# Kernel tuning notes

Measured on AMD Instinct MI355X. Metric: run time of the kernel, lower is better.

## Reference

```python
import jax, jax.numpy as jnp
import numpy as np

B, S, D = 16, 1024, 768
H = 12
HD = D // H  # 64


def setup_inputs() -> dict:
    key = jax.random.key(0)
    ks = jax.random.split(key, 9)
    s = 1.0 / np.sqrt(D)
    x = jax.random.normal(ks[0], (B, S, D), dtype=jnp.float32)
    Wq = jax.random.uniform(ks[1], (H, HD, D), minval=-s, maxval=s, dtype=jnp.float32)
    bq = jax.random.uniform(ks[2], (H, HD), minval=-s, maxval=s, dtype=jnp.float32)
    Wk = jax.random.uniform(ks[3], (H, HD, D), minval=-s, maxval=s, dtype=jnp.float32)
    bk = jax.random.uniform(ks[4], (H, HD), minval=-s, maxval=s, dtype=jnp.float32)
    Wv = jax.random.uniform(ks[5], (H, HD, D), minval=-s, maxval=s, dtype=jnp.float32)
    bv = jax.random.uniform(ks[6], (H, HD), minval=-s, maxval=s, dtype=jnp.float32)
    Wo = jax.random.uniform(ks[7], (D, D), minval=-s, maxval=s, dtype=jnp.float32)
    bo = jax.random.uniform(ks[8], (D,), minval=-s, maxval=s, dtype=jnp.float32)
    return {"x": x, "Wq": Wq, "bq": bq, "Wk": Wk, "bk": bk,
            "Wv": Wv, "bv": bv, "Wo": Wo, "bo": bo}


def reference(x, Wq, bq, Wk, bk, Wv, bv, Wo, bo):
    # per-head projections: [B,S,D] x [H,HD,D] -> [B,H,S,HD]
    q = jnp.einsum('bsd,hed->bhse', x, Wq) + bq[None, :, None, :]
    k = jnp.einsum('bsd,hed->bhse', x, Wk) + bk[None, :, None, :]
    v = jnp.einsum('bsd,hed->bhse', x, Wv) + bv[None, :, None, :]
    scores = jnp.einsum('bhse,bhte->bhst', q, k) / jnp.sqrt(jnp.float32(HD))
    weights = jax.nn.softmax(scores, axis=-1)  # [B,H,S,S]
    attn = jnp.einsum('bhst,bhte->bhse', weights, v)  # [B,H,S,HD]
    # concat heads along last dim (head order matches torch.cat)
    concat = attn.transpose(0, 2, 1, 3).reshape(B, S, H * HD)
    out = concat @ Wo.T + bo
    return out
```

## Files before the change

kernel.cpp:

```cpp
#include <hip/hip_runtime.h>
#include <hip/hip_bf16.h>

typedef unsigned short u16;
typedef unsigned int u32;
typedef __attribute__((ext_vector_type(2))) unsigned int u32x2;
typedef __attribute__((ext_vector_type(4))) unsigned int u32x4;
typedef __attribute__((ext_vector_type(4))) float f32x4;
typedef __attribute__((ext_vector_type(16))) float f32x16;
typedef __attribute__((ext_vector_type(8))) short s16x8;
typedef __attribute__((ext_vector_type(4))) unsigned short u16x4;
typedef __attribute__((ext_vector_type(8))) unsigned short u16x8;

#define QSCALE 0.18033688011112042f

#define BARRIER() do { __builtin_amdgcn_s_barrier(); __builtin_amdgcn_sched_barrier(0); } while (0)
#define WAIT_VM0() do { asm volatile("s_waitcnt vmcnt(0)" ::: "memory"); __builtin_amdgcn_sched_barrier(0); } while (0)

__device__ inline u16 f2bf(float f) {
  union { float f; unsigned u; } x; x.f = f;
  unsigned r = x.u + 0x7FFFu + ((x.u >> 16) & 1u);
  return (u16)(r >> 16);
}

__device__ inline u32 cvtpk(float lo, float hi) {
  u32 r;
  asm("v_cvt_pk_bf16_f32 %0, %1, %2" : "=v"(r) : "v"(lo), "v"(hi));
  return r;
}

__device__ inline void pl32swap(u32& a, u32& b) {
  asm("v_permlane32_swap_b32 %0, %1" : "+v"(a), "+v"(b));
}

__global__ void cvt_all(const float* __restrict__ x,
                        const float* __restrict__ Wq, const float* __restrict__ Wk,
                        const float* __restrict__ Wv, const float* __restrict__ Wo,
                        const float* __restrict__ bq, const float* __restrict__ bk,
                        const float* __restrict__ bv,
                        u16* __restrict__ xb, u16* __restrict__ wqkv,
                        u16* __restrict__ wo, float* __restrict__ bqkv) {
  int i = blockIdx.x * blockDim.x + threadIdx.x;
  const int NX = 3145728;
  const int NW = 147456;
  if (i < NX) {
    const float4 v = ((const float4*)x)[i];
    u16x4 o; o[0] = f2bf(v.x); o[1] = f2bf(v.y); o[2] = f2bf(v.z); o[3] = f2bf(v.w);
    ((u16x4*)xb)[i] = o;
    return;
  }
  i -= NX;
  if (i < 4 * NW) {
    const int w = i / NW, k = i - w * NW;
    const float* s = (w == 0) ? Wq : (w == 1) ? Wk : (w == 2) ? Wv : Wo;
    u16* d = (w == 3) ? wo : wqkv + (size_t)w * 589824;
    const float4 v = ((const float4*)s)[k];
    u16x4 o; o[0] = f2bf(v.x); o[1] = f2bf(v.y); o[2] = f2bf(v.z); o[3] = f2bf(v.w);
    ((u16x4*)d)[k] = o;
    return;
  }
  i -= 4 * NW;
  if (i < 576) {
    const int w = i / 192, k = i - w * 192;
    const float* s = (w == 0) ? bq : (w == 1) ? bk : bv;
    ((float4*)bqkv)[w * 192 + k] = ((const float4*)s)[k];
  }
}

template<int FC, int STORE_BF16, int QKV_SCALE, int WV>
__global__ __launch_bounds__(512, 2) void gemm8(
    const u16* __restrict__ A, const u16* __restrict__ Bm,
    const float* __restrict__ bias, void* __restrict__ C,
    u16* __restrict__ vt,
    int N, int K, int ntiles)
{
  constexpr int ASZ = 32768;
  constexpr int BSZ = FC * 8192;
  constexpr int BUF = ASZ + BSZ;
  __shared__ char lds[2 * BUF];

  const int tid = threadIdx.x, wave = tid >> 6, lane = tid & 63;
  const int il = lane & 15, g = lane >> 4;
  const int Lr = lane >> 3, Lc = lane & 7;
  const int wm = wave >> 2, wn = wave & 3;

  const int cpx = (int)gridDim.x >> 3;
  const int orig = (blockIdx.x & 7) * cpx + (blockIdx.x >> 3);
  const int tm = (orig / ntiles) * 256, tn = (orig % ntiles) * (FC * 64);

  const size_t Kb = (size_t)K * 2;
  const int colb = (Lc * 16) ^ (Lr << 4);

  auto stageAll = [&](int buf, int k0) {
    char* base = &lds[buf * BUF];
#pragma unroll
    for (int c = 0; c < 4; ++c) {
      const int row = tm + c * 64 + wave * 8 + Lr;
      const char* src = (const char*)A + (size_t)row * Kb + k0 * 2 + colb;
      __builtin_amdgcn_global_load_lds((const __attribute__((address_space(1))) void*)src,
          (__attribute__((address_space(3))) void*)(base + c * 8192 + wave * 1024), 16, 0, 0);
    }
#pragma unroll
    for (int c = 0; c < FC; ++c) {
      const int row = tn + c * 64 + wave * 8 + Lr;
      const char* src = (const char*)Bm + (size_t)row * Kb + k0 * 2 + colb;
      __builtin_amdgcn_global_load_lds((const __attribute__((address_space(1))) void*)src,
          (__attribute__((address_space(3))) void*)(base + ASZ + c * 8192 + wave * 1024), 16, 0, 0);
    }
  };
  auto ldA = [&](int buf, int fr, int kk) -> s16x8 {
    const int row = wm * 128 + fr * 16 + il;
    const int cb = (kk * 64 + g * 16) ^ ((il & 7) << 4);
    return *(const s16x8*)&lds[buf * BUF + row * 128 + cb];
  };
  auto ldB = [&](int buf, int fc, int kk) -> s16x8 {
    const int row = wn * (FC * 16) + fc * 16 + il;
    const int cb = (kk * 64 + g * 16) ^ ((il & 7) << 4);
    return *(const s16x8*)&lds[buf * BUF + ASZ + row * 128 + cb];
  };

  f32x4 acc[8][FC] = {};
  const int nK = K >> 6;

  stageAll(0, 0);
  WAIT_VM0();
  BARRIER();

  for (int t = 0; t < nK; ++t) {
    const int cur = t & 1;
    const bool pf = (t + 1 < nK);
    if (pf) stageAll(cur ^ 1, (t + 1) << 6);

    s16x8 bfr[FC][2];
#pragma unroll
    for (int fc = 0; fc < FC; ++fc) { bfr[fc][0] = ldB(cur, fc, 0); bfr[fc][1] = ldB(cur, fc, 1); }

#pragma unroll
    for (int p = 0; p < 4; ++p) {
      s16x8 a00 = ldA(cur, 2 * p, 0),     a01 = ldA(cur, 2 * p, 1);
      s16x8 a10 = ldA(cur, 2 * p + 1, 0), a11 = ldA(cur, 2 * p + 1, 1);
      __builtin_amdgcn_s_setprio(1);
#pragma unroll
      for (int fc = 0; fc < FC; ++fc) {
        acc[2*p][fc]   = __builtin_amdgcn_mfma_f32_16x16x32_bf16(a00, bfr[fc][0], acc[2*p][fc], 0, 0, 0);
        acc[2*p][fc]   = __builtin_amdgcn_mfma_f32_16x16x32_bf16(a01, bfr[fc][1], acc[2*p][fc], 0, 0, 0);
        acc[2*p+1][fc] = __builtin_amdgcn_mfma_f32_16x16x32_bf16(a10, bfr[fc][0], acc[2*p+1][fc], 0, 0, 0);
        acc[2*p+1][fc] = __builtin_amdgcn_mfma_f32_16x16x32_bf16(a11, bfr[fc][1], acc[2*p+1][fc], 0, 0, 0);
      }
      __builtin_amdgcn_s_setprio(0);
    }
    if (pf) WAIT_VM0();
    BARRIER();
  }

  if (WV && tn >= 1536) {
#pragma unroll
    for (int fr = 0; fr < 8; ++fr) {
      const int row0 = tm + wm * 128 + fr * 16 + g * 4;
      const int bb_ = row0 >> 10, s0 = row0 & 1023;
#pragma unroll
      for (int fc = 0; fc < FC; ++fc) {
        const int hcol = tn + wn * (FC * 16) + fc * 16 + il - 1536;
        const float bb = bias[hcol + 1536];
        u16x4 o;
#pragma unroll
        for (int r = 0; r < 4; ++r) o[r] = f2bf(acc[fr][fc][r] + bb);
        *(u16x4*)(vt + ((size_t)(bb_ * 12 + (hcol >> 6)) * 64 + (hcol & 63)) * 1024 + s0) = o;
      }
    }
    return;
  }
#pragma unroll
  for (int fr = 0; fr < 8; ++fr) {
    const int row0 = tm + wm * 128 + fr * 16 + g * 4;
#pragma unroll
    for (int fc = 0; fc < FC; ++fc) {
      const int col = tn + wn * (FC * 16) + fc * 16 + il;
      const float bb = bias[col];
#pragma unroll
      for (int r = 0; r < 4; ++r) {
        float v = acc[fr][fc][r] + bb;
        if (QKV_SCALE) { if (col < 768) v *= QSCALE; }
        if (STORE_BF16) ((u16*)C)[(size_t)(row0 + r) * N + col] = f2bf(v);
        else            ((float*)C)[(size_t)(row0 + r) * N + col] = v;
      }
    }
  }
}

__global__ __launch_bounds__(256) void attn_fwd(const u16* __restrict__ qkv,
                                                const u16* __restrict__ vT,
                                                u16* __restrict__ concat)
{
  __shared__ u16 Kl[64 * 64];
  __shared__ u16 Vl[64 * 64];

  const int tid = threadIdx.x, wave = tid >> 6, lane = tid & 63;
  const int wg = blockIdx.x;
  const int bh = (wg & 7) | ((wg >> 6) << 3);
  const int qb = (wg >> 3) & 7;
  const int b = bh / 12, h = bh % 12;
  const int q = lane & 31, hi = lane >> 5;
  const int qs0 = qb * 128 + wave * 32;

  const char* qkvB = (const char*)qkv;
  const size_t rowB = (size_t)b * 1024 * 4608;
  const char* vtB = (const char*)vT + (size_t)bh * 64 * 2048;

  s16x8 qf[4];
  {
    const char* qp = qkvB + rowB + (size_t)(qs0 + q) * 4608 + h * 128 + hi * 16;
#pragma unroll
    for (int s = 0; s < 4; ++s) qf[s] = *(const s16x8*)(qp + s * 32);
  }

  float l_ = 0.f;
  f32x16 accO[2] = {};

  const int Lr = lane >> 3, Lc = lane & 7;
  const int colb = (Lc * 16) ^ ((Lr & 7) << 4);
  const int swk = (q & 7) << 4;

  for (int kv0 = 0; kv0 < 1024; kv0 += 64) {
#pragma unroll
    for (int i = 0; i < 2; ++i) {
      const int row = wave * 16 + i * 8 + Lr;
      const char* ks = qkvB + rowB + (size_t)(kv0 + row) * 4608 + 1536 + h * 128 + colb;
      __builtin_amdgcn_global_load_lds((const __attribute__((address_space(1))) void*)ks,
          (__attribute__((address_space(3))) void*)(Kl + (wave * 16 + i * 8) * 64), 16, 0, 0);
      const char* vs = vtB + (size_t)row * 2048 + kv0 * 2 + colb;
      __builtin_amdgcn_global_load_lds((const __attribute__((address_space(1))) void*)vs,
          (__attribute__((address_space(3))) void*)(Vl + (wave * 16 + i * 8) * 64), 16, 0, 0);
    }
    __syncthreads();

    f32x16 st[2] = {};
    __builtin_amdgcn_s_setprio(1);
#pragma unroll
    for (int s = 0; s < 4; ++s) {
      const int cb = (s * 32 + hi * 16) ^ swk;
      s16x8 k0 = *(const s16x8*)((const char*)Kl + q * 128 + cb);
      s16x8 k1 = *(const s16x8*)((const char*)Kl + (32 + q) * 128 + cb);
      st[0] = __builtin_amdgcn_mfma_f32_32x32x16_bf16(k0, qf[s], st[0], 0, 0, 0);
      st[1] = __builtin_amdgcn_mfma_f32_32x32x16_bf16(k1, qf[s], st[1], 0, 0, 0);
    }
    __builtin_amdgcn_s_setprio(0);

    float cs0 = 0.f, cs1 = 0.f;
#pragma unroll
    for (int r = 0; r < 16; ++r) {
      const float p0 = __builtin_amdgcn_exp2f(st[0][r]);
      const float p1 = __builtin_amdgcn_exp2f(st[1][r]);
      st[0][r] = p0; st[1][r] = p1;
      cs0 += p0; cs1 += p1;
    }
    l_ += cs0 + cs1;

    s16x8 pa[4];
#pragma unroll
    for (int kb = 0; kb < 2; ++kb)
#pragma unroll
      for (int ks = 0; ks < 2; ++ks) {
        u32 A0 = cvtpk(st[kb][ks * 8 + 0], st[kb][ks * 8 + 1]);
        u32 A1 = cvtpk(st[kb][ks * 8 + 2], st[kb][ks * 8 + 3]);
        u32 B0 = cvtpk(st[kb][ks * 8 + 4], st[kb][ks * 8 + 5]);
        u32 B1 = cvtpk(st[kb][ks * 8 + 6], st[kb][ks * 8 + 7]);
        pl32swap(A0, B0);
        pl32swap(A1, B1);
        u32x4 w = {A0, A1, B0, B1};
        pa[kb * 2 + ks] = __builtin_bit_cast(s16x8, w);
      }

    __builtin_amdgcn_s_setprio(1);
#pragma unroll
    for (int ksub = 0; ksub < 4; ++ksub) {
      const int cb = (ksub * 32 + hi * 16) ^ swk;
      s16x8 v0 = *(const s16x8*)((const char*)Vl + q * 128 + cb);
      s16x8 v1 = *(const s16x8*)((const char*)Vl + (32 + q) * 128 + cb);
      accO[0] = __builtin_amdgcn_mfma_f32_32x32x16_bf16(v0, pa[ksub], accO[0], 0, 0, 0);
      accO[1] = __builtin_amdgcn_mfma_f32_32x32x16_bf16(v1, pa[ksub], accO[1], 0, 0, 0);
    }
    __builtin_amdgcn_s_setprio(0);
    __syncthreads();
  }

  l_ += __shfl_xor(l_, 32);
  const float linv = __builtin_amdgcn_rcpf(l_);
  u16* crow = concat + ((size_t)b * 1024 + qs0 + q) * 768 + h * 64;
#pragma unroll
  for (int eb = 0; eb < 2; ++eb)
#pragma unroll
    for (int rq = 0; rq < 4; ++rq) {
      u32 w0 = cvtpk(accO[eb][rq * 4 + 0] * linv, accO[eb][rq * 4 + 1] * linv);
      u32 w1 = cvtpk(accO[eb][rq * 4 + 2] * linv, accO[eb][rq * 4 + 3] * linv);
      u32x2 w = {w0, w1};
      *(u16x4*)(crow + eb * 32 + rq * 8 + hi * 4) = __builtin_bit_cast(u16x4, w);
    }
}

extern "C" void kernel_launch(void* const* d_in, const int* in_sizes, int n_in,
                              void* d_out, int out_size, void* d_ws, size_t ws_size,
                              hipStream_t stream) {
  const float* x  = (const float*)d_in[0];
  const float* Wq = (const float*)d_in[1];
  const float* bq = (const float*)d_in[2];
  const float* Wk = (const float*)d_in[3];
  const float* bk = (const float*)d_in[4];
  const float* Wv = (const float*)d_in[5];
  const float* bv = (const float*)d_in[6];
  const float* Wo = (const float*)d_in[7];
  const float* bo = (const float*)d_in[8];

  const size_t XN = (size_t)16384 * 768;
  const size_t WN = (size_t)768 * 768;

  u16* xb   = (u16*)d_ws;
  u16* wqkv = xb + XN;
  u16* wo   = wqkv + 3 * WN;
  float* bqkv = (float*)(wo + WN);
  u16* qkv  = (u16*)(bqkv + 2304);
  u16* vt   = qkv + (size_t)16384 * 2304;
  u16* cc   = xb;

  cvt_all<<<(3736128 + 255) / 256, 256, 0, stream>>>(
      x, Wq, Wk, Wv, Wo, bq, bk, bv, xb, wqkv, wo, bqkv);

  gemm8<3, 1, 1, 1><<<768, 512, 0, stream>>>(xb, wqkv, bqkv, qkv, vt, 2304, 768, 12);

  attn_fwd<<<1536, 256, 0, stream>>>(qkv, vt, cc);

  gemm8<3, 0, 0, 0><<<256, 512, 0, stream>>>(cc, wo, bo, d_out, nullptr, 768, 768, 4);
}
```

Before: 182.0 us.

## Switch attention to 16x16 MFMA tiles with LDS-staged P and more workgroups

Rewrites the attention kernel so each wave owns 16 query rows instead of 32, using 16x16x32 bf16 MFMAs instead of 32x32x16. The P matrix now goes through a per-wave LDS buffer rather than being rearranged with permlane32 swaps, and the grid doubles to 3072 workgroups with a remapped block index and launch bounds asking for 8 blocks per CU. The goal is lower register use and higher occupancy so latency is better hidden. The cost is that K/V tiles are loaded twice as often per query, plus extra LDS traffic and round trips for P.

Result: slower. 189.1 us (+3.9%).

```diff
diff --git a/kernel.cpp b/kernel.cpp
--- a/kernel.cpp
+++ b/kernel.cpp
@@ -26,10 +26,6 @@
   u32 r;
   asm("v_cvt_pk_bf16_f32 %0, %1, %2" : "=v"(r) : "v"(lo), "v"(hi));
   return r;
-}
-
-__device__ inline void pl32swap(u32& a, u32& b) {
-  asm("v_permlane32_swap_b32 %0, %1" : "+v"(a), "+v"(b));
 }
 
 __global__ void cvt_all(const float* __restrict__ x,
@@ -187,38 +183,40 @@
   }
 }
 
-__global__ __launch_bounds__(256) void attn_fwd(const u16* __restrict__ qkv,
-                                                const u16* __restrict__ vT,
-                                                u16* __restrict__ concat)
+__global__ __launch_bounds__(256, 8) void attn_fwd(const u16* __restrict__ qkv,
+                                                   const u16* __restrict__ vT,
+                                                   u16* __restrict__ concat)
 {
   __shared__ u16 Kl[64 * 64];
   __shared__ u16 Vl[64 * 64];
+  __shared__ u16 Pl[4][16 * 64];
 
   const int tid = threadIdx.x, wave = tid >> 6, lane = tid & 63;
   const int wg = blockIdx.x;
-  const int bh = (wg & 7) | ((wg >> 6) << 3);
-  const int qb = (wg >> 3) & 7;
+  const int orig = (wg & 7) * 384 + (wg >> 3);
+  const int bh = orig >> 4, qb = orig & 15;
   const int b = bh / 12, h = bh % 12;
-  const int q = lane & 31, hi = lane >> 5;
-  const int qs0 = qb * 128 + wave * 32;
+  const int il = lane & 15, g = lane >> 4;
+  const int qs0 = qb * 64 + wave * 16;
 
   const char* qkvB = (const char*)qkv;
   const size_t rowB = (size_t)b * 1024 * 4608;
   const char* vtB = (const char*)vT + (size_t)bh * 64 * 2048;
-
-  s16x8 qf[4];
+  char* PlB = (char*)&Pl[wave][0];
+
+  s16x8 qf0, qf1;
   {
-    const char* qp = qkvB + rowB + (size_t)(qs0 + q) * 4608 + h * 128 + hi * 16;
-#pragma unroll
-    for (int s = 0; s < 4; ++s) qf[s] = *(const s16x8*)(qp + s * 32);
+    const char* qp = qkvB + rowB + (size_t)(qs0 + il) * 4608 + h * 128 + g * 16;
+    qf0 = *(const s16x8*)qp;
+    qf1 = *(const s16x8*)(qp + 64);
   }
 
   float l_ = 0.f;
-  f32x16 accO[2] = {};
+  f32x4 accO[4] = {};
 
   const int Lr = lane >> 3, Lc = lane & 7;
   const int colb = (Lc * 16) ^ ((Lr & 7) << 4);
-  const int swk = (q & 7) << 4;
+  const int swk = (il & 7) << 4;
 
   for (int kv0 = 0; kv0 < 1024; kv0 += 64) {
 #pragma unroll
@@ -233,68 +231,59 @@
     }
     __syncthreads();
 
-    f32x16 st[2] = {};
+#pragma unroll
+    for (int h2 = 0; h2 < 2; ++h2) {
+      f32x4 st0 = {}, st1 = {};
+      __builtin_amdgcn_s_setprio(1);
+#pragma unroll
+      for (int kk = 0; kk < 2; ++kk) {
+        const int cb = (kk * 64 + g * 16) ^ swk;
+        s16x8 k0 = *(const s16x8*)((const char*)Kl + (h2 * 32 + il) * 128 + cb);
+        s16x8 k1 = *(const s16x8*)((const char*)Kl + (h2 * 32 + 16 + il) * 128 + cb);
+        st0 = __builtin_amdgcn_mfma_f32_16x16x32_bf16(k0, (kk ? qf1 : qf0), st0, 0, 0, 0);
+        st1 = __builtin_amdgcn_mfma_f32_16x16x32_bf16(k1, (kk ? qf1 : qf0), st1, 0, 0, 0);
+      }
+      __builtin_amdgcn_s_setprio(0);
+
+      float cs = 0.f;
+#pragma unroll
+      for (int r = 0; r < 4; ++r) {
+        st0[r] = __builtin_amdgcn_exp2f(st0[r]);
+        st1[r] = __builtin_amdgcn_exp2f(st1[r]);
+        cs += st0[r] + st1[r];
+      }
+      l_ += cs;
+
+      u32x2 w0 = {cvtpk(st0[0], st0[1]), cvtpk(st0[2], st0[3])};
+      u32x2 w1 = {cvtpk(st1[0], st1[1]), cvtpk(st1[2], st1[3])};
+      *(u32x2*)(PlB + il * 128 + ((h2 * 64 + g * 8) ^ swk)) = w0;
+      *(u32x2*)(PlB + il * 128 + ((h2 * 64 + 32 + g * 8) ^ swk)) = w1;
+    }
+
+    s16x8 pf0 = *(const s16x8*)(PlB + il * 128 + ((g * 16) ^ swk));
+    s16x8 pf1 = *(const s16x8*)(PlB + il * 128 + ((64 + g * 16) ^ swk));
     __builtin_amdgcn_s_setprio(1);
 #pragma unroll
-    for (int s = 0; s < 4; ++s) {
-      const int cb = (s * 32 + hi * 16) ^ swk;
-      s16x8 k0 = *(const s16x8*)((const char*)Kl + q * 128 + cb);
-      s16x8 k1 = *(const s16x8*)((const char*)Kl + (32 + q) * 128 + cb);
-      st[0] = __builtin_amdgcn_mfma_f32_32x32x16_bf16(k0, qf[s], st[0], 0, 0, 0);
-      st[1] = __builtin_amdgcn_mfma_f32_32x32x16_bf16(k1, qf[s], st[1], 0, 0, 0);
-    }
-    __builtin_amdgcn_s_setprio(0);
-
-    float cs0 = 0.f, cs1 = 0.f;
-#pragma unroll
-    for (int r = 0; r < 16; ++r) {
-      const float p0 = __builtin_amdgcn_exp2f(st[0][r]);
-      const float p1 = __builtin_amdgcn_exp2f(st[1][r]);
-      st[0][r] = p0; st[1][r] = p1;
-      cs0 += p0; cs1 += p1;
-    }
-    l_ += cs0 + cs1;
-
-    s16x8 pa[4];
-#pragma unroll
-    for (int kb = 0; kb < 2; ++kb)
-#pragma unroll
-      for (int ks = 0; ks < 2; ++ks) {
-        u32 A0 = cvtpk(st[kb][ks * 8 + 0], st[kb][ks * 8 + 1]);
-        u32 A1 = cvtpk(st[kb][ks * 8 + 2], st[kb][ks * 8 + 3]);
-        u32 B0 = cvtpk(st[kb][ks * 8 + 4], st[kb][ks * 8 + 5]);
-        u32 B1 = cvtpk(st[kb][ks * 8 + 6], st[kb][ks * 8 + 7]);
-        pl32swap(A0, B0);
-        pl32swap(A1, B1);
-        u32x4 w = {A0, A1, B0, B1};
-        pa[kb * 2 + ks] = __builtin_bit_cast(s16x8, w);
-      }
-
-    __builtin_amdgcn_s_setprio(1);
-#pragma unroll
-    for (int ksub = 0; ksub < 4; ++ksub) {
-      const int cb = (ksub * 32 + hi * 16) ^ swk;
-      s16x8 v0 = *(const s16x8*)((const char*)Vl + q * 128 + cb);
-      s16x8 v1 = *(const s16x8*)((const char*)Vl + (32 + q) * 128 + cb);
-      accO[0] = __builtin_amdgcn_mfma_f32_32x32x16_bf16(v0, pa[ksub], accO[0], 0, 0, 0);
-      accO[1] = __builtin_amdgcn_mfma_f32_32x32x16_bf16(v1, pa[ksub], accO[1], 0, 0, 0);
+    for (int mt = 0; mt < 4; ++mt) {
+      s16x8 v0 = *(const s16x8*)((const char*)Vl + (mt * 16 + il) * 128 + ((g * 16) ^ swk));
+      s16x8 v1 = *(const s16x8*)((const char*)Vl + (mt * 16 + il) * 128 + ((64 + g * 16) ^ swk));
+      accO[mt] = __builtin_amdgcn_mfma_f32_16x16x32_bf16(v0, pf0, accO[mt], 0, 0, 0);
+      accO[mt] = __builtin_amdgcn_mfma_f32_16x16x32_bf16(v1, pf1, accO[mt], 0, 0, 0);
     }
     __builtin_amdgcn_s_setprio(0);
     __syncthreads();
   }
 
+  l_ += __shfl_xor(l_, 16);
   l_ += __shfl_xor(l_, 32);
   const float linv = __builtin_amdgcn_rcpf(l_);
-  u16* crow = concat + ((size_t)b * 1024 + qs0 + q) * 768 + h * 64;
-#pragma unroll
-  for (int eb = 0; eb < 2; ++eb)
-#pragma unroll
-    for (int rq = 0; rq < 4; ++rq) {
-      u32 w0 = cvtpk(accO[eb][rq * 4 + 0] * linv, accO[eb][rq * 4 + 1] * linv);
-      u32 w1 = cvtpk(accO[eb][rq * 4 + 2] * linv, accO[eb][rq * 4 + 3] * linv);
-      u32x2 w = {w0, w1};
-      *(u16x4*)(crow + eb * 32 + rq * 8 + hi * 4) = __builtin_bit_cast(u16x4, w);
-    }
+  u16* crow = concat + ((size_t)b * 1024 + qs0 + il) * 768 + h * 64;
+#pragma unroll
+  for (int mt = 0; mt < 4; ++mt) {
+    u32x2 w = {cvtpk(accO[mt][0] * linv, accO[mt][1] * linv),
+               cvtpk(accO[mt][2] * linv, accO[mt][3] * linv)};
+    *(u16x4*)(crow + mt * 16 + g * 4) = __builtin_bit_cast(u16x4, w);
+  }
 }
 
 extern "C" void kernel_launch(void* const* d_in, const int* in_sizes, int n_in,
@@ -326,7 +315,7 @@
 
   gemm8<3, 1, 1, 1><<<768, 512, 0, stream>>>(xb, wqkv, bqkv, qkv, vt, 2304, 768, 12);
 
-  attn_fwd<<<1536, 256, 0, stream>>>(qkv, vt, cc);
+  attn_fwd<<<3072, 256, 0, stream>>>(qkv, vt, cc);
 
   gemm8<3, 0, 0, 0><<<256, 512, 0, stream>>>(cc, wo, bo, d_out, nullptr, 768, 768, 4);
 }
```
